# Performance work log

Hardware: AMD Instinct MI355X
Metric: run time of the kernel (lower is better)

Reference implementation:

```python
import jax, jax.numpy as jnp
from jax import lax
import numpy as np

B, C_IN, C_OUT, T, N, E = 4, 32, 32, 48, 2000, 16000


def _tconv(x, w, b):
    # Conv2d with kernel (3,1), padding (1,0): temporal conv over T, per-node.
    y = lax.conv_general_dilated(x, w, window_strides=(1, 1),
                                 padding=((1, 1), (0, 0)),
                                 dimension_numbers=('NCHW', 'OIHW', 'NCHW'))
    return y + b[None, :, None, None]


def setup_inputs() -> dict:
    key = jax.random.key(0)
    ks = jax.random.split(key, 8)
    x = jax.random.normal(ks[0], (B, C_IN, T, N), dtype=jnp.float32)
    edge_index = jax.random.randint(ks[1], (2, E), 0, N, dtype=jnp.int64)
    w1 = jax.random.normal(ks[2], (C_OUT, C_IN, 3, 1), dtype=jnp.float32) * 0.05
    b1 = jnp.zeros((C_OUT,), dtype=jnp.float32)
    gcn_w = jax.random.normal(ks[3], (C_OUT, C_OUT), dtype=jnp.float32) * 0.05
    gcn_b = jnp.zeros((C_OUT,), dtype=jnp.float32)
    w2 = jax.random.normal(ks[4], (C_OUT, C_OUT, 3, 1), dtype=jnp.float32) * 0.05
    b2 = jnp.zeros((C_OUT,), dtype=jnp.float32)
    return {"x": x, "edge_index": edge_index, "w1": w1, "b1": b1,
            "gcn_w": gcn_w, "gcn_b": gcn_b, "w2": w2, "b2": b2}


def reference(x, edge_index, w1, b1, gcn_w, gcn_b, w2, b2):
    # temporal conv 1 + relu
    h = jax.nn.relu(_tconv(x, w1, b1))          # [B, C, T, N]
    Bs, C, Ts, Ns = h.shape
    # replicate-graph GCN: same edge_index for all B*T graphs
    xf = h.transpose(0, 2, 3, 1).reshape(Bs * Ts, Ns, C)   # [BT, N, C]
    xw = xf @ gcn_w                                        # linear transform first
    src, dst = edge_index[0], edge_index[1]
    # GCN symmetric normalization with self-loops: deg = 1 + in-degree
    deg = jnp.zeros((Ns,), xw.dtype).at[dst].add(1.0) + 1.0
    dinv = lax.rsqrt(deg)
    wedge = dinv[src] * dinv[dst]                           # [E]

    def aggregate(g):  # g: [N, C] for one graph
        return jnp.zeros((Ns, C), g.dtype).at[dst].add(g[src] * wedge[:, None])

    agg = jax.vmap(aggregate)(xw)                           # [BT, N, C]
    out = agg + (1.0 / deg)[None, :, None] * xw + gcn_b     # self-loop term + bias
    out = out.reshape(Bs, Ts, Ns, C).transpose(0, 3, 1, 2)  # [B, C, T, N]
    # temporal conv 2
    return _tconv(out, w2, b2)
```

## Files before the change

### kernel.cpp

```cpp
#include <hip/hip_runtime.h>

#define BB 4
#define CIN 32
#define COUT 32
#define TT 48
#define NN 2000
#define EE 16000
#define BT (BB*TT)
#define PADCOL 24576


__global__ __launch_bounds__(256) void k_zero(int* __restrict__ col,
                                              float* __restrict__ wedge,
                                              int* __restrict__ gcnt) {
    int i = blockIdx.x * 256 + threadIdx.x;
    if (i < PADCOL) { col[i] = 0; wedge[i] = 0.f; }
    if (i < 2048)   gcnt[i] = 0;
}


__global__ __launch_bounds__(256) void k_count(const int* __restrict__ ei,
                                               int* __restrict__ gcnt) {
    int e = blockIdx.x * 256 + threadIdx.x;
    if (e < EE) atomicAdd(&gcnt[ei[EE + e]], 1);
}


__global__ __launch_bounds__(256) void k_wprep(
        const float* __restrict__ w1, const float* __restrict__ gw,
        const float* __restrict__ gb, const float* __restrict__ w2,
        const float* __restrict__ cb2,
        float* __restrict__ w1t, float* __restrict__ w2c,
        float* __restrict__ biasE) {
    int i = blockIdx.x * 256 + threadIdx.x;
    if (i < 3072) {
        int c = i & 31, r = i >> 5;
        int co = r & 31, k = r >> 5;
        w1t[i] = w1[c * 96 + co * 3 + k];
        float acc = 0.f;
#pragma unroll
        for (int q = 0; q < 32; q++)
            acc += gw[co * 32 + q] * w2[c * 96 + q * 3 + k];
        w2c[i] = acc;
    } else if (i < 3168) {
        int j = i - 3072;
        int cls = j >> 5, c = j & 31;
        float bk0 = 0.f, bk1 = 0.f, bk2 = 0.f;
#pragma unroll
        for (int co = 0; co < 32; co++) {
            float g = gb[co];
            bk0 += g * w2[c * 96 + co * 3 + 0];
            bk1 += g * w2[c * 96 + co * 3 + 1];
            bk2 += g * w2[c * 96 + co * 3 + 2];
        }
        float v = cb2[c] + bk1;
        if (cls != 0) v += bk0;
        if (cls != 2) v += bk2;
        biasE[j] = v;
    }
}


__global__ __launch_bounds__(1024) void k_build(
        const int* __restrict__ gcnt,
        int* __restrict__ rowptr, float* __restrict__ dinv2,
        float* __restrict__ dinvg, int* __restrict__ fillptr) {
    __shared__ int cnt[2048];
    __shared__ int buf[2048];
    int t = threadIdx.x;

    cnt[t] = gcnt[t]; cnt[t + 1024] = gcnt[t + 1024];
    __syncthreads();

    for (int i = t; i < 2048; i += 1024)
        buf[i] = (i < NN) ? ((cnt[i] + 3) & ~3) : 0;
    __syncthreads();
    for (int s = 1; s < 2048; s <<= 1) {
        int i0 = t, i1 = t + 1024;
        int a0 = buf[i0] + ((i0 >= s) ? buf[i0 - s] : 0);
        int a1 = buf[i1] + ((i1 >= s) ? buf[i1 - s] : 0);
        __syncthreads();
        buf[i0] = a0; buf[i1] = a1;
        __syncthreads();
    }

    for (int i = t; i < 2048; i += 1024) {
        if (i < NN) {
            rowptr[i + 1] = buf[i];
            float deg = (float)(cnt[i] + 1);
            dinvg[i] = rsqrtf(deg);
            dinv2[i] = 1.0f / deg;
            fillptr[i] = buf[i] - ((cnt[i] + 3) & ~3);
        }
    }
    if (t == 0) rowptr[0] = 0;
}


__global__ void k_fill(const int* __restrict__ ei, int* __restrict__ fillptr,
                       const float* __restrict__ dinvg,
                       int* __restrict__ col, float* __restrict__ wedge) {
    int e = blockIdx.x * blockDim.x + threadIdx.x;
    if (e < EE) {
        int s = ei[e], d = ei[EE + e];
        int pos = atomicAdd(fillptr + d, 1);
        col[pos]   = s;
        wedge[pos] = dinvg[s] * dinvg[d];
    }
}


__global__ __launch_bounds__(256) void k_conv1(const float* __restrict__ x,
                                               const float* __restrict__ w1t,
                                               const float* __restrict__ b1,
                                               float* __restrict__ hbuf) {
    int bid = blockIdx.x;
    int xcd = bid & 7;
    int i   = bid >> 3;
    int nch = i & 7;
    int r   = i >> 3;
    int tloc = r % 6, b = r / 6;
    int t = xcd * 6 + tloc;
    int n = nch * 256 + threadIdx.x;
    if (n >= NN) return;
    int g = b * TT + t;
    int gb = g >> 3, gsub = g & 7;

    float ha[COUT];
#pragma unroll
    for (int c = 0; c < COUT; c++) ha[c] = b1[c];

    const float* xbase = x + ((size_t)b * CIN * TT) * NN + n;
    bool hasL = (t > 0), hasR = (t < TT - 1);
    const float* pL = xbase + (size_t)(hasL ? t - 1 : 0) * NN;
    const float* pM = xbase + (size_t)t * NN;
    const float* pR = xbase + (size_t)(hasR ? t + 1 : 0) * NN;

    float xa[CIN], xm[CIN];
#pragma unroll
    for (int ci = 0; ci < CIN; ci++) xa[ci] = pL[(size_t)ci * TT * NN];
#pragma unroll
    for (int ci = 0; ci < CIN; ci++) xm[ci] = pM[(size_t)ci * TT * NN];
    __builtin_amdgcn_sched_barrier(0);

    if (hasL) {
        const float* wp = w1t;
#pragma unroll
        for (int ci = 0; ci < CIN; ci++) {
#pragma unroll
            for (int c = 0; c < COUT; c++) ha[c] += xa[ci] * wp[ci * COUT + c];
        }
    }
    __builtin_amdgcn_sched_barrier(0);

#pragma unroll
    for (int ci = 0; ci < CIN; ci++) xa[ci] = pR[(size_t)ci * TT * NN];
    __builtin_amdgcn_sched_barrier(0);

    {
        const float* wp = w1t + 1024;
#pragma unroll
        for (int ci = 0; ci < CIN; ci++) {
#pragma unroll
            for (int c = 0; c < COUT; c++) ha[c] += xm[ci] * wp[ci * COUT + c];
        }
    }
    __builtin_amdgcn_sched_barrier(0);

    if (hasR) {
        const float* wp = w1t + 2048;
#pragma unroll
        for (int ci = 0; ci < CIN; ci++) {
#pragma unroll
            for (int c = 0; c < COUT; c++) ha[c] += xa[ci] * wp[ci * COUT + c];
        }
    }

    float4* pa = (float4*)(hbuf + (((size_t)gb * NN + n) * 8 + gsub) * 32);
#pragma unroll
    for (int q = 0; q < 8; q++)
        pa[q] = make_float4(fmaxf(ha[4*q], 0.f), fmaxf(ha[4*q+1], 0.f),
                            fmaxf(ha[4*q+2], 0.f), fmaxf(ha[4*q+3], 0.f));
}


__global__ __launch_bounds__(256) void k_agg(const float* __restrict__ hbuf,
                                             const int* __restrict__ rowptr,
                                             const int* __restrict__ col,
                                             const float* __restrict__ wedge,
                                             const float* __restrict__ dinv2,
                                             float* __restrict__ gbuf) {
    int bid = blockIdx.x;
    int xcd = bid & 7;
    int q   = bid >> 3;
    int gbr = q / 500;
    int nch = q % 500;
    int gb  = gbr * 8 + xcd;
    int wid  = threadIdx.x >> 6;
    int lane = threadIdx.x & 63;
    int gsub = lane >> 3;
    int cq   = lane & 7;
    int n    = nch * 4 + wid;

    const float* xg = hbuf + (size_t)gb * NN * 256;
    size_t loff = (size_t)gsub * 32 + cq * 4;

    float4 self = *(const float4*)(xg + (size_t)n * 256 + loff);
    float dv = dinv2[n];
    float4 acc = make_float4(dv * self.x, dv * self.y, dv * self.z, dv * self.w);

    int j  = rowptr[n];
    int je = rowptr[n + 1];
    for (; j < je; j += 4) {
        int4   cc = *(const int4*)(col + j);
        float4 ww = *(const float4*)(wedge + j);
        float4 v0 = *(const float4*)(xg + (size_t)cc.x * 256 + loff);
        float4 v1 = *(const float4*)(xg + (size_t)cc.y * 256 + loff);
        float4 v2 = *(const float4*)(xg + (size_t)cc.z * 256 + loff);
        float4 v3 = *(const float4*)(xg + (size_t)cc.w * 256 + loff);
        acc.x += ww.x*v0.x + ww.y*v1.x + ww.z*v2.x + ww.w*v3.x;
        acc.y += ww.x*v0.y + ww.y*v1.y + ww.z*v2.y + ww.w*v3.y;
        acc.z += ww.x*v0.z + ww.y*v1.z + ww.z*v2.z + ww.w*v3.z;
        acc.w += ww.x*v0.w + ww.y*v1.w + ww.z*v2.w + ww.w*v3.w;
    }

    int g = gb * 8 + gsub;
    *(float4*)(gbuf + ((size_t)g * NN + n) * 32 + cq * 4) = acc;
}


#define LD32(GV, GP) { \
    _Pragma("unroll") \
    for (int q_ = 0; q_ < 8; q_++) { \
        float4 v_ = (GP)[q_]; \
        GV[4*q_] = v_.x; GV[4*q_+1] = v_.y; GV[4*q_+2] = v_.z; GV[4*q_+3] = v_.w; } }

#define FMA32(ACC, GV, WP) { \
    _Pragma("unroll") \
    for (int cm_ = 0; cm_ < 32; cm_++) { \
        float g_ = GV[cm_]; \
        _Pragma("unroll") \
        for (int c_ = 0; c_ < 32; c_++) ACC[c_] += g_ * (WP)[cm_ * 32 + c_]; } }

__global__ __launch_bounds__(256) void k_conv2(const float* __restrict__ gbuf,
                                               const float* __restrict__ w2c,
                                               const float* __restrict__ biasE,
                                               float* __restrict__ out) {
    int bid  = blockIdx.x;
    int xcd  = bid & 7;
    int slot = bid >> 3;
    int grp  = xcd * 24 + (slot >> 3);
    int nch  = slot & 7;
    int b = grp / TT;
    int t = grp % TT;
    int n = nch * 256 + threadIdx.x;
    if (n >= NN) return;

    bool hasL = (t > 0), hasR = (t < TT - 1);
    const float4* pL = (const float4*)(gbuf + (((size_t)(b * TT + (hasL ? t - 1 : 0))) * NN + n) * CIN);
    const float4* pM = (const float4*)(gbuf + (((size_t)(b * TT + t)) * NN + n) * CIN);
    const float4* pR = (const float4*)(gbuf + (((size_t)(b * TT + (hasR ? t + 1 : 0))) * NN + n) * CIN);

    float o[COUT];
#pragma unroll
    for (int c = 0; c < COUT; c++) o[c] = 0.f;

    float ga[CIN], gm[CIN];
    LD32(ga, pL);
    LD32(gm, pM);
    __builtin_amdgcn_sched_barrier(0);

    if (hasL) { FMA32(o, ga, w2c); }
    __builtin_amdgcn_sched_barrier(0);

    LD32(ga, pR);
    __builtin_amdgcn_sched_barrier(0);

    FMA32(o, gm, w2c + 1024);
    __builtin_amdgcn_sched_barrier(0);

    if (hasR) { FMA32(o, ga, w2c + 2048); }

    int cls = (t == 0) ? 0 : ((t == TT - 1) ? 2 : 1);
    const float* bp = biasE + cls * 32;
#pragma unroll
    for (int c = 0; c < COUT; c++)
        out[(((size_t)b * COUT + c) * TT + t) * NN + n] = o[c] + bp[c];
}


extern "C" void kernel_launch(void* const* d_in, const int* in_sizes, int n_in,
                              void* d_out, int out_size, void* d_ws, size_t ws_size,
                              hipStream_t stream) {
    const float* x     = (const float*)d_in[0];
    const int*   ei    = (const int*)d_in[1];
    const float* w1    = (const float*)d_in[2];
    const float* b1    = (const float*)d_in[3];
    const float* gcn_w = (const float*)d_in[4];
    const float* gcn_b = (const float*)d_in[5];
    const float* w2    = (const float*)d_in[6];
    const float* b2    = (const float*)d_in[7];
    float* out = (float*)d_out;

    const size_t XWB = (size_t)BT * NN * COUT * sizeof(float);
    char* w = (char*)d_ws;
    float* hbuf    = (float*)w;  w += XWB;
    float* gbuf    = (float*)w;  w += XWB;
    int*   rowptr  = (int*)w;    w += 8192;
    float* dinv2   = (float*)w;  w += 8192;
    float* dinvg   = (float*)w;  w += 8192;
    int*   fillptr = (int*)w;    w += 8192;
    int*   gcnt    = (int*)w;    w += 8192;
    int*   col     = (int*)w;    w += PADCOL * sizeof(int);
    float* wedge   = (float*)w;  w += PADCOL * sizeof(float);
    float* w1t     = (float*)w;  w += 3072 * sizeof(float);
    float* w2c     = (float*)w;  w += 3072 * sizeof(float);
    float* biasE   = (float*)w;  w += 96 * sizeof(float);

    k_zero <<<dim3((PADCOL + 255) / 256), dim3(256), 0, stream>>>(col, wedge, gcnt);
    k_count<<<dim3((EE + 255) / 256), dim3(256), 0, stream>>>(ei, gcnt);
    k_wprep<<<dim3(13), dim3(256), 0, stream>>>(w1, gcn_w, gcn_b, w2, b2,
                                                w1t, w2c, biasE);
    k_build<<<dim3(1), dim3(1024), 0, stream>>>(gcnt, rowptr, dinv2, dinvg, fillptr);
    k_fill <<<dim3((EE + 255) / 256), dim3(256), 0, stream>>>(ei, fillptr, dinvg, col, wedge);
    k_conv1<<<dim3(1536), dim3(256), 0, stream>>>(x, w1t, b1, hbuf);
    k_agg  <<<dim3(12000), dim3(256), 0, stream>>>(hbuf, rowptr, col, wedge, dinv2, gbuf);
    k_conv2<<<dim3(1536), dim3(256), 0, stream>>>(gbuf, w2c, biasE, out);
}
```

Before: 232.1 us.

## Merge zero and weight-prep kernels, wave-shuffle scan, smaller conv1 blocks

Folds the buffer-zeroing and weight-preparation kernels into one launch, which drops one kernel launch from the preprocessing chain. The single-block prefix scan over node degrees now uses wavefront shuffles plus a small per-wave offset table instead of a shared-memory Hillis-Steele scan with many barriers. conv1 is launched as twice as many 128-thread blocks, so fewer threads sit idle at the tail of the node range. The aim is lower launch and sync overhead in the serial setup kernels.

```diff
diff --git a/kernel.cpp b/kernel.cpp
--- a/kernel.cpp
+++ b/kernel.cpp
@@ -10,29 +10,22 @@
 #define PADCOL 24576
 
 
-__global__ __launch_bounds__(256) void k_zero(int* __restrict__ col,
-                                              float* __restrict__ wedge,
-                                              int* __restrict__ gcnt) {
-    int i = blockIdx.x * 256 + threadIdx.x;
-    if (i < PADCOL) { col[i] = 0; wedge[i] = 0.f; }
-    if (i < 2048)   gcnt[i] = 0;
-}
-
-
-__global__ __launch_bounds__(256) void k_count(const int* __restrict__ ei,
-                                               int* __restrict__ gcnt) {
-    int e = blockIdx.x * 256 + threadIdx.x;
-    if (e < EE) atomicAdd(&gcnt[ei[EE + e]], 1);
-}
-
-
-__global__ __launch_bounds__(256) void k_wprep(
+__global__ __launch_bounds__(256) void k_pre(
+        int* __restrict__ col, float* __restrict__ wedge,
+        int* __restrict__ gcnt,
         const float* __restrict__ w1, const float* __restrict__ gw,
         const float* __restrict__ gb, const float* __restrict__ w2,
         const float* __restrict__ cb2,
         float* __restrict__ w1t, float* __restrict__ w2c,
         float* __restrict__ biasE) {
-    int i = blockIdx.x * 256 + threadIdx.x;
+    int bid = blockIdx.x;
+    if (bid < 96) {
+        int i = bid * 256 + threadIdx.x;
+        col[i] = 0; wedge[i] = 0.f;
+        if (i < 2048) gcnt[i] = 0;
+        return;
+    }
+    int i = (bid - 96) * 256 + threadIdx.x;
     if (i < 3072) {
         int c = i & 31, r = i >> 5;
         int co = r & 31, k = r >> 5;
@@ -61,37 +54,58 @@
 }
 
 
+__global__ __launch_bounds__(256) void k_count(const int* __restrict__ ei,
+                                               int* __restrict__ gcnt) {
+    int e = blockIdx.x * 256 + threadIdx.x;
+    if (e < EE) atomicAdd(&gcnt[ei[EE + e]], 1);
+}
+
+
 __global__ __launch_bounds__(1024) void k_build(
         const int* __restrict__ gcnt,
         int* __restrict__ rowptr, float* __restrict__ dinv2,
         float* __restrict__ dinvg, int* __restrict__ fillptr) {
-    __shared__ int cnt[2048];
-    __shared__ int buf[2048];
+    __shared__ int wtot[16], woff[16];
     int t = threadIdx.x;
-
-    cnt[t] = gcnt[t]; cnt[t + 1024] = gcnt[t + 1024];
+    int i0 = 2 * t, i1 = 2 * t + 1;
+    int c0 = (i0 < NN) ? gcnt[i0] : 0;
+    int c1 = (i1 < NN) ? gcnt[i1] : 0;
+    int a0 = (i0 < NN) ? ((c0 + 3) & ~3) : 0;
+    int a1 = (i1 < NN) ? ((c1 + 3) & ~3) : 0;
+
+    int lane = t & 63, w = t >> 6;
+    int s = a0 + a1;
+#pragma unroll
+    for (int d = 1; d < 64; d <<= 1) {
+        int v = __shfl_up(s, d, 64);
+        if (lane >= d) s += v;
+    }
+    if (lane == 63) wtot[w] = s;
     __syncthreads();
-
-    for (int i = t; i < 2048; i += 1024)
-        buf[i] = (i < NN) ? ((cnt[i] + 3) & ~3) : 0;
+    if (t == 0) {
+        int run = 0;
+#pragma unroll
+        for (int k = 0; k < 16; k++) { woff[k] = run; run += wtot[k]; }
+    }
     __syncthreads();
-    for (int s = 1; s < 2048; s <<= 1) {
-        int i0 = t, i1 = t + 1024;
-        int a0 = buf[i0] + ((i0 >= s) ? buf[i0 - s] : 0);
-        int a1 = buf[i1] + ((i1 >= s) ? buf[i1 - s] : 0);
-        __syncthreads();
-        buf[i0] = a0; buf[i1] = a1;
-        __syncthreads();
-    }
-
-    for (int i = t; i < 2048; i += 1024) {
-        if (i < NN) {
-            rowptr[i + 1] = buf[i];
-            float deg = (float)(cnt[i] + 1);
-            dinvg[i] = rsqrtf(deg);
-            dinv2[i] = 1.0f / deg;
-            fillptr[i] = buf[i] - ((cnt[i] + 3) & ~3);
-        }
+
+    int incl = woff[w] + s;
+    int b1v = incl;
+    int b0v = incl - a1;
+
+    if (i0 < NN) {
+        rowptr[i0 + 1] = b0v;
+        float deg = (float)(c0 + 1);
+        dinvg[i0] = rsqrtf(deg);
+        dinv2[i0] = 1.0f / deg;
+        fillptr[i0] = b0v - a0;
+    }
+    if (i1 < NN) {
+        rowptr[i1 + 1] = b1v;
+        float deg = (float)(c1 + 1);
+        dinvg[i1] = rsqrtf(deg);
+        dinv2[i1] = 1.0f / deg;
+        fillptr[i1] = b1v - a1;
     }
     if (t == 0) rowptr[0] = 0;
 }
@@ -110,18 +124,18 @@
 }
 
 
-__global__ __launch_bounds__(256) void k_conv1(const float* __restrict__ x,
+__global__ __launch_bounds__(128) void k_conv1(const float* __restrict__ x,
                                                const float* __restrict__ w1t,
                                                const float* __restrict__ b1,
                                                float* __restrict__ hbuf) {
     int bid = blockIdx.x;
     int xcd = bid & 7;
     int i   = bid >> 3;
-    int nch = i & 7;
-    int r   = i >> 3;
+    int nch = i & 15;
+    int r   = i >> 4;
     int tloc = r % 6, b = r / 6;
     int t = xcd * 6 + tloc;
-    int n = nch * 256 + threadIdx.x;
+    int n = nch * 128 + threadIdx.x;
     if (n >= NN) return;
     int g = b * TT + t;
     int gb = g >> 3, gsub = g & 7;
@@ -317,13 +331,13 @@
     float* w2c     = (float*)w;  w += 3072 * sizeof(float);
     float* biasE   = (float*)w;  w += 96 * sizeof(float);
 
-    k_zero <<<dim3((PADCOL + 255) / 256), dim3(256), 0, stream>>>(col, wedge, gcnt);
+    k_pre  <<<dim3(109), dim3(256), 0, stream>>>(col, wedge, gcnt,
+                                                 w1, gcn_w, gcn_b, w2, b2,
+                                                 w1t, w2c, biasE);
     k_count<<<dim3((EE + 255) / 256), dim3(256), 0, stream>>>(ei, gcnt);
-    k_wprep<<<dim3(13), dim3(256), 0, stream>>>(w1, gcn_w, gcn_b, w2, b2,
-                                                w1t, w2c, biasE);
     k_build<<<dim3(1), dim3(1024), 0, stream>>>(gcnt, rowptr, dinv2, dinvg, fillptr);
     k_fill <<<dim3((EE + 255) / 256), dim3(256), 0, stream>>>(ei, fillptr, dinvg, col, wedge);
-    k_conv1<<<dim3(1536), dim3(256), 0, stream>>>(x, w1t, b1, hbuf);
+    k_conv1<<<dim3(3072), dim3(128), 0, stream>>>(x, w1t, b1, hbuf);
     k_agg  <<<dim3(12000), dim3(256), 0, stream>>>(hbuf, rowptr, col, wedge, dinv2, gbuf);
     k_conv2<<<dim3(1536), dim3(256), 0, stream>>>(gbuf, w2c, biasE, out);
 }
```

After: 230.3 us. Within noise of the previous version (-0.7%).
